# Kernel optimization log

Measured on AMD Instinct MI355X. Metric: run time of the kernel, lower is better.

## Reference

```python
import jax, jax.numpy as jnp
import numpy as np

B, T, S, C, F = 32, 50, 2048, 8, 32  # batch, time, spatial steps, in-channels, filters
K, STRIDE = 2, 2
DN = ('NWC', 'WIO', 'NWC')


def hard_sigmoid(x):
    # TF-Keras hard_sigmoid: clip(0.2*x + 0.5, 0, 1)
    return jnp.clip(0.2 * x + 0.5, 0.0, 1.0)


def setup_inputs() -> dict:
    key = jax.random.key(0)
    ks = jax.random.split(key, 5)
    x = jax.random.normal(ks[0], (B, T, S, C), jnp.float32)
    kernel = jax.random.normal(ks[1], (K, C, 4 * F), jnp.float32) * 0.05
    rec_kernel = jax.random.normal(ks[2], (K, F, 4 * F), jnp.float32) * 0.05
    bias = jnp.zeros((4 * F,), jnp.float32)
    dense_w = jax.random.normal(ks[3], ((S // STRIDE) * F, 1), jnp.float32) * 0.02
    dense_b = jnp.zeros((1,), jnp.float32)
    return dict(x=x, kernel=kernel, rec_kernel=rec_kernel, bias=bias,
                dense_w=dense_w, dense_b=dense_b)


def reference(x, kernel, rec_kernel, bias, dense_w, dense_b):
    b, t, s, c = x.shape
    f = rec_kernel.shape[1]
    # Input convolution for all timesteps at once (stride 2, SAME padding)
    xc = jax.lax.conv_general_dilated(x.reshape(b * t, s, c), kernel,
                                      (STRIDE,), 'SAME', dimension_numbers=DN)
    xc = xc + bias
    sh = xc.shape[1]  # ceil(s / stride)
    xc = xc.reshape(b, t, sh, 4 * f).transpose(1, 0, 2, 3)  # time-major for scan

    def step(carry, xt):
        h, cst = carry
        hc = jax.lax.conv_general_dilated(h, rec_kernel, (1,), 'SAME',
                                          dimension_numbers=DN)
        z = xt + hc
        zi, zf, zc, zo = jnp.split(z, 4, axis=-1)
        i = hard_sigmoid(zi)
        fg = hard_sigmoid(zf)
        cst = fg * cst + i * jnp.tanh(zc)
        o = hard_sigmoid(zo)
        h = o * jnp.tanh(cst)
        return (h, cst), None

    h0 = jnp.zeros((b, sh, f), x.dtype)
    (h, _), _ = jax.lax.scan(step, (h0, h0), xc)
    # Flatten + Dense(1)
    return h.reshape(b, -1) @ dense_w + dense_b
```

## Files before the change

kernel.cpp:

```cpp
#include <hip/hip_runtime.h>


#define TT 50
#define LTILE 64
#define ROWS 129
#define HSTR 40

typedef __attribute__((ext_vector_type(8))) short short8;
typedef __attribute__((ext_vector_type(4))) float floatx4;

__device__ __forceinline__ float b2f_hi(unsigned short s) {
  union { float f; unsigned u; } v; v.u = ((unsigned)s) << 16; return v.f;
}
__device__ __forceinline__ unsigned short f2b_rne(float f) {
  union { float f; unsigned u; } v; v.f = f;
  unsigned r = v.u + 0x7FFFu + ((v.u >> 16) & 1u);
  return (unsigned short)(r >> 16);
}
__device__ __forceinline__ unsigned short f2b_trunc(float f) {
  union { float f; unsigned u; } v; v.f = f;
  return (unsigned short)(v.u >> 16);
}
__device__ __forceinline__ float hsig(float x) {
  return __builtin_amdgcn_fmed3f(__builtin_fmaf(0.2f, x, 0.5f), 0.0f, 1.0f);
}
__device__ __forceinline__ float ftanh(float x) {
  float e = __expf(2.0f * x);
  return 1.0f - 2.0f * __builtin_amdgcn_rcpf(e + 1.0f);
}

__global__ __launch_bounds__(256, 2)
void convlstm_scan(const float* __restrict__ xs,
                   const float* __restrict__ ks,
                   const float* __restrict__ rks,
                   const float* __restrict__ bs,
                   const float* __restrict__ dws,
                   float* __restrict__ acc_out) {
  __shared__ short hbH[2][ROWS * HSTR];
  __shared__ short hbL[2][ROWS * HSTR];

  const int tid  = threadIdx.x;
  const int b    = blockIdx.x >> 4;
  const int j0   = (blockIdx.x & 15) * LTILE;
  const int wave = tid >> 6;
  const int lane = tid & 63;
  const int q    = lane >> 4;
  const int f0   = lane & 15;

  for (int e = tid; e < ROWS * HSTR; e += 256) {
    ((int*)hbH)[e] = 0;
    ((int*)hbL)[e] = 0;
  }

  short8 Bwh0[8], Bwh1[8], Bxw[8];
#pragma unroll
  for (int n = 0; n < 8; ++n) {
    const int oc = n * 16 + f0;
    short8 th;
#pragma unroll
    for (int j = 0; j < 8; ++j)
      th[j] = (short)f2b_rne(rks[(q * 8 + j) * 128 + oc]);
    Bwh0[n] = th;
#pragma unroll
    for (int j = 0; j < 8; ++j)
      th[j] = (short)f2b_rne(rks[(32 + q * 8 + j) * 128 + oc]);
    Bwh1[n] = th;
    short8 tx = {0, 0, 0, 0, 0, 0, 0, 0};
    if (q < 2) {
#pragma unroll
      for (int j = 0; j < 8; ++j)
        tx[j] = (short)f2b_rne(ks[(q * 8 + j) * 128 + oc]);
    } else if (q == 2) {
      tx[0] = (short)f2b_rne(bs[oc]);
    }
    Bxw[n] = tx;
  }

  short8 axc = {0, 0, 0, 0, 0, 0, 0, 0};
  if (q == 2) axc[0] = (short)0x3F80;

  const floatx4 zero4 = {0.0f, 0.0f, 0.0f, 0.0f};

  float cst[2][8];
#pragma unroll
  for (int s = 0; s < 2; ++s)
#pragma unroll
    for (int i = 0; i < 8; ++i) cst[s][i] = 0.0f;

  floatx4 px0[2], px1[2];
#pragma unroll
  for (int s = 0; s < 2; ++s) {
    const int jr = (wave + 4 * s) * 16 + f0;
    const int jm = min(j0 + jr, 1023);
    const float* xp = xs + (size_t)b * TT * (2048 * 8) +
                      (size_t)(2 * jm + (q & 1)) * 8;
    px0[s] = *(const floatx4*)xp;
    px1[s] = *(const floatx4*)(xp + 4);
  }

  const int maxrows = 1024 - j0;
  __syncthreads();

  for (int t = 0; t < TT; ++t) {
    const short* curH = hbH[t & 1];
    const short* curL = hbL[t & 1];
    short* nxtH = hbH[(t & 1) ^ 1];
    short* nxtL = hbL[(t & 1) ^ 1];
    int rows = LTILE + (TT - 1) - t;
    if (rows > maxrows) rows = maxrows;
    const int nmt = (rows + 15) >> 4;
    const int act1 = (wave + 4) < nmt;
    const int tn = (t < TT - 1) ? t + 1 : t;
    const float* xnext = xs + ((size_t)(b * TT + tn)) * (2048 * 8);

    short8 a0h[2], a0l[2], a1h[2], a1l[2];
#pragma unroll
    for (int s = 0; s < 2; ++s) {
      const int jr = (wave + 4 * s) * 16 + f0;
      a0h[s] = *(const short8*)&curH[jr * HSTR + q * 8];
      a0l[s] = *(const short8*)&curL[jr * HSTR + q * 8];
      a1h[s] = *(const short8*)&curH[(jr + 1) * HSTR + q * 8];
      a1l[s] = *(const short8*)&curL[(jr + 1) * HSTR + q * 8];
    }

    short8 ax[2];
#pragma unroll
    for (int s = 0; s < 2; ++s) {
      ax[s] = axc;
      if (q < 2) {
        floatx4 x0 = px0[s], x1 = px1[s];
#pragma unroll
        for (int jj = 0; jj < 4; ++jj) ax[s][jj] = (short)f2b_trunc(x0[jj]);
#pragma unroll
        for (int jj = 0; jj < 4; ++jj) ax[s][4 + jj] = (short)f2b_trunc(x1[jj]);
      }
    }

#pragma unroll
    for (int s = 0; s < 2; ++s) {
      const int jr = (wave + 4 * s) * 16 + f0;
      const int jm = min(j0 + jr, 1023);
      const float* xp = xnext + (size_t)(2 * jm + (q & 1)) * 8;
      px0[s] = *(const floatx4*)xp;
      px1[s] = *(const floatx4*)(xp + 4);
    }

#pragma unroll
    for (int s = 0; s < 2; ++s) {
      if (s == 1 && !act1) continue;
      const int m = wave + 4 * s;

      floatx4 acc[8];
#pragma unroll
      for (int n = 0; n < 8; ++n)
        acc[n] = __builtin_amdgcn_mfma_f32_16x16x32_bf16(ax[s], Bxw[n], zero4, 0, 0, 0);
#pragma unroll
      for (int n = 0; n < 8; ++n)
        acc[n] = __builtin_amdgcn_mfma_f32_16x16x32_bf16(a0h[s], Bwh0[n], acc[n], 0, 0, 0);
#pragma unroll
      for (int n = 0; n < 8; ++n)
        acc[n] = __builtin_amdgcn_mfma_f32_16x16x32_bf16(a1h[s], Bwh1[n], acc[n], 0, 0, 0);
#pragma unroll
      for (int n = 0; n < 8; ++n)
        acc[n] = __builtin_amdgcn_mfma_f32_16x16x32_bf16(a0l[s], Bwh0[n], acc[n], 0, 0, 0);
#pragma unroll
      for (int n = 0; n < 8; ++n)
        acc[n] = __builtin_amdgcn_mfma_f32_16x16x32_bf16(a1l[s], Bwh1[n], acc[n], 0, 0, 0);

      const int jw = m * 16 + q * 4;
#pragma unroll
      for (int p = 0; p < 2; ++p) {
#pragma unroll
        for (int r = 0; r < 4; ++r) {
          float zi = acc[0 + p][r], zf = acc[2 + p][r];
          float zc = acc[4 + p][r], zo = acc[6 + p][r];
          float ig = hsig(zi), fg = hsig(zf), og = hsig(zo);
          float cs = cst[s][p * 4 + r];
          float cn = __builtin_fmaf(fg, cs, ig * ftanh(zc));
          cst[s][p * 4 + r] = cn;
          float hv = og * ftanh(cn);
          union { float f; unsigned u; } v; v.f = hv;
          unsigned hiu = v.u & 0xFFFF0000u;
          union { float f; unsigned u; } w; w.u = hiu;
          float rem = hv - w.f;
          nxtH[(jw + r) * HSTR + p * 16 + f0] = (short)(hiu >> 16);
          nxtL[(jw + r) * HSTR + p * 16 + f0] = (short)f2b_trunc(rem);
        }
      }
    }
    __syncthreads();
  }

  const short* hH = hbH[0];
  const short* hL = hbL[0];
  float part = 0.0f;
  for (int e = tid; e < LTILE * 32; e += 256) {
    int jr = e >> 5, f = e & 31;
    float hv = b2f_hi((unsigned short)hH[jr * HSTR + f]) +
               b2f_hi((unsigned short)hL[jr * HSTR + f]);
    part += hv * dws[(j0 + jr) * 32 + f];
  }
#pragma unroll
  for (int off = 32; off > 0; off >>= 1) part += __shfl_down(part, off);
  if (lane == 0) atomicAdd(&acc_out[b], part);
}

__global__ void init_acc(float* ws) {
  if (threadIdx.x < 32) ws[threadIdx.x] = 0.0f;
}

__global__ void finalize(const float* __restrict__ ws,
                         const float* __restrict__ db,
                         float* __restrict__ out) {
  int i = threadIdx.x;
  if (i < 32) out[i] = ws[i] + db[0];
}

extern "C" void kernel_launch(void* const* d_in, const int* in_sizes, int n_in,
                              void* d_out, int out_size, void* d_ws, size_t ws_size,
                              hipStream_t stream) {
  const float* x  = (const float*)d_in[0];
  const float* k  = (const float*)d_in[1];
  const float* rk = (const float*)d_in[2];
  const float* bi = (const float*)d_in[3];
  const float* dw = (const float*)d_in[4];
  const float* db = (const float*)d_in[5];
  float* ws = (float*)d_ws;
  float* out = (float*)d_out;

  hipLaunchKernelGGL(init_acc, dim3(1), dim3(64), 0, stream, ws);
  hipLaunchKernelGGL(convlstm_scan, dim3(512), dim3(256), 0, stream,
                     x, k, rk, bi, dw, ws);
  hipLaunchKernelGGL(finalize, dim3(1), dim3(64), 0, stream, ws, db, out);
}
```

Before: 259.5 us.

## Drop split-bf16 hidden state, pack h stores, fuse dense into last step

The hidden state was stored as a bf16 high part plus a bf16 residual. That costs two extra passes of 8 MFMAs per tile, a second LDS buffer and extra LDS reads and writes every step. This change keeps a single round-to-nearest bf16 copy of h. It also permutes gate output channels so each lane stores two adjacent filters as one 32-bit word. The Flatten plus Dense(1) reduction moves into the final time step, using fp32 h directly and removing the separate epilogue pass over LDS. The cost is lower precision in the recurrent matmul inputs, which may increase numerical error over 50 steps.

```diff
diff --git a/kernel.cpp b/kernel.cpp
--- a/kernel.cpp
+++ b/kernel.cpp
@@ -9,9 +9,6 @@
 typedef __attribute__((ext_vector_type(8))) short short8;
 typedef __attribute__((ext_vector_type(4))) float floatx4;
 
-__device__ __forceinline__ float b2f_hi(unsigned short s) {
-  union { float f; unsigned u; } v; v.u = ((unsigned)s) << 16; return v.f;
-}
 __device__ __forceinline__ unsigned short f2b_rne(float f) {
   union { float f; unsigned u; } v; v.f = f;
   unsigned r = v.u + 0x7FFFu + ((v.u >> 16) & 1u);
@@ -37,7 +34,6 @@
                    const float* __restrict__ dws,
                    float* __restrict__ acc_out) {
   __shared__ short hbH[2][ROWS * HSTR];
-  __shared__ short hbL[2][ROWS * HSTR];
 
   const int tid  = threadIdx.x;
   const int b    = blockIdx.x >> 4;
@@ -47,15 +43,13 @@
   const int q    = lane >> 4;
   const int f0   = lane & 15;
 
-  for (int e = tid; e < ROWS * HSTR; e += 256) {
+  for (int e = tid; e < ROWS * HSTR; e += 256)
     ((int*)hbH)[e] = 0;
-    ((int*)hbL)[e] = 0;
-  }
 
   short8 Bwh0[8], Bwh1[8], Bxw[8];
 #pragma unroll
   for (int n = 0; n < 8; ++n) {
-    const int oc = n * 16 + f0;
+    const int oc = (n >> 1) * 32 + 2 * f0 + (n & 1);
     short8 th;
 #pragma unroll
     for (int j = 0; j < 8; ++j)
@@ -99,28 +93,26 @@
   }
 
   const int maxrows = 1024 - j0;
+  float part = 0.0f;
   __syncthreads();
 
   for (int t = 0; t < TT; ++t) {
     const short* curH = hbH[t & 1];
-    const short* curL = hbL[t & 1];
     short* nxtH = hbH[(t & 1) ^ 1];
-    short* nxtL = hbL[(t & 1) ^ 1];
     int rows = LTILE + (TT - 1) - t;
     if (rows > maxrows) rows = maxrows;
     const int nmt = (rows + 15) >> 4;
     const int act1 = (wave + 4) < nmt;
-    const int tn = (t < TT - 1) ? t + 1 : t;
+    const int last = (t == TT - 1);
+    const int tn = last ? t : t + 1;
     const float* xnext = xs + ((size_t)(b * TT + tn)) * (2048 * 8);
 
-    short8 a0h[2], a0l[2], a1h[2], a1l[2];
+    short8 a0h[2], a1h[2];
 #pragma unroll
     for (int s = 0; s < 2; ++s) {
       const int jr = (wave + 4 * s) * 16 + f0;
       a0h[s] = *(const short8*)&curH[jr * HSTR + q * 8];
-      a0l[s] = *(const short8*)&curL[jr * HSTR + q * 8];
       a1h[s] = *(const short8*)&curH[(jr + 1) * HSTR + q * 8];
-      a1l[s] = *(const short8*)&curL[(jr + 1) * HSTR + q * 8];
     }
 
     short8 ax[2];
@@ -160,46 +152,35 @@
 #pragma unroll
       for (int n = 0; n < 8; ++n)
         acc[n] = __builtin_amdgcn_mfma_f32_16x16x32_bf16(a1h[s], Bwh1[n], acc[n], 0, 0, 0);
-#pragma unroll
-      for (int n = 0; n < 8; ++n)
-        acc[n] = __builtin_amdgcn_mfma_f32_16x16x32_bf16(a0l[s], Bwh0[n], acc[n], 0, 0, 0);
-#pragma unroll
-      for (int n = 0; n < 8; ++n)
-        acc[n] = __builtin_amdgcn_mfma_f32_16x16x32_bf16(a1l[s], Bwh1[n], acc[n], 0, 0, 0);
 
       const int jw = m * 16 + q * 4;
 #pragma unroll
-      for (int p = 0; p < 2; ++p) {
-#pragma unroll
-        for (int r = 0; r < 4; ++r) {
+      for (int r = 0; r < 4; ++r) {
+        float hv2[2];
+#pragma unroll
+        for (int p = 0; p < 2; ++p) {
           float zi = acc[0 + p][r], zf = acc[2 + p][r];
           float zc = acc[4 + p][r], zo = acc[6 + p][r];
           float ig = hsig(zi), fg = hsig(zf), og = hsig(zo);
           float cs = cst[s][p * 4 + r];
           float cn = __builtin_fmaf(fg, cs, ig * ftanh(zc));
           cst[s][p * 4 + r] = cn;
-          float hv = og * ftanh(cn);
-          union { float f; unsigned u; } v; v.f = hv;
-          unsigned hiu = v.u & 0xFFFF0000u;
-          union { float f; unsigned u; } w; w.u = hiu;
-          float rem = hv - w.f;
-          nxtH[(jw + r) * HSTR + p * 16 + f0] = (short)(hiu >> 16);
-          nxtL[(jw + r) * HSTR + p * 16 + f0] = (short)f2b_trunc(rem);
+          hv2[p] = og * ftanh(cn);
+        }
+        if (!last) {
+          unsigned pk = (unsigned)f2b_rne(hv2[0]) |
+                        ((unsigned)f2b_rne(hv2[1]) << 16);
+          *(unsigned*)&nxtH[(jw + r) * HSTR + 2 * f0] = pk;
+        } else {
+          const int di = (j0 + jw + r) * 32 + 2 * f0;
+          part = __builtin_fmaf(hv2[0], dws[di],
+                 __builtin_fmaf(hv2[1], dws[di + 1], part));
         }
       }
     }
     __syncthreads();
   }
 
-  const short* hH = hbH[0];
-  const short* hL = hbL[0];
-  float part = 0.0f;
-  for (int e = tid; e < LTILE * 32; e += 256) {
-    int jr = e >> 5, f = e & 31;
-    float hv = b2f_hi((unsigned short)hH[jr * HSTR + f]) +
-               b2f_hi((unsigned short)hL[jr * HSTR + f]);
-    part += hv * dws[(j0 + jr) * 32 + f];
-  }
 #pragma unroll
   for (int off = 32; off > 0; off >>= 1) part += __shfl_down(part, off);
   if (lane == 0) atomicAdd(&acc_out[b], part);
```

After: 241.0 us. -7.1%, faster.
